# Kernel tuning notes

Hardware: AMD Instinct MI355X
Metric: run time of the kernel (lower is better)

## Reference

```python
import jax, jax.numpy as jnp
import numpy as np

L, T, R = 2, 2, 2          # layers, node types (0=user,1=movie), edge types
NU, NM, E = 50000, 10000, 500000
C, H, DPHI = 128, 4, 64
D = C // H                 # head dim = 32
SQRT_D = float(np.sqrt(D))


def setup_inputs() -> dict:
    key = jax.random.key(0)
    ks = jax.random.split(key, 16)
    s = 0.05
    src = jax.random.randint(ks[0], (E,), 0, NU)
    dst = jax.random.randint(ks[1], (E,), 0, NM)
    return {
        "user_emb": jax.random.normal(ks[2], (NU, C)) * 0.01,
        "movie_emb": jax.random.normal(ks[3], (NM, C)) * 0.01,
        "phi": jax.random.normal(ks[4], (NM, DPHI)),
        "meta_w": jax.random.normal(ks[5], (DPHI, C)) * s,
        "meta_b": jnp.zeros((C,)),
        "kw": jax.random.normal(ks[6], (L, T, C, C)) * s,
        "kb": jnp.zeros((L, T, C)),
        "qw": jax.random.normal(ks[7], (L, T, C, C)) * s,
        "qb": jnp.zeros((L, T, C)),
        "vw": jax.random.normal(ks[8], (L, T, C, C)) * s,
        "vb": jnp.zeros((L, T, C)),
        "a_rel": jax.random.normal(ks[9], (L, R, H, D, D)) * s,
        "m_rel": jax.random.normal(ks[10], (L, R, H, D, D)) * s,
        "p_rel": jnp.ones((L, R, H)),
        "ow": jax.random.normal(ks[11], (L, T, C, C)) * s,
        "ob": jnp.zeros((L, T, C)),
        "skip": jnp.ones((L, T)),
        "edge_index": jnp.stack([src, dst]),  # [2,E], row0=user idx, row1=movie idx
    }


def _segment_softmax(logits, seg, n):
    # logits: [E,H], seg: [E] destination node ids
    m = jax.ops.segment_max(logits, seg, num_segments=n)
    e = jnp.exp(logits - m[seg])
    s = jax.ops.segment_sum(e, seg, num_segments=n)
    return e / (s[seg] + 1e-16)


def _hgt_layer(xs, kw, kb, qw, qb, vw, vb, a_rel, m_rel, p_rel, ow, ob, skip, edge_index):
    ns = [x.shape[0] for x in xs]
    k = [(xs[t] @ kw[t] + kb[t]).reshape(ns[t], H, D) for t in range(T)]
    q = [(xs[t] @ qw[t] + qb[t]).reshape(ns[t], H, D) for t in range(T)]
    v = [(xs[t] @ vw[t] + vb[t]).reshape(ns[t], H, D) for t in range(T)]
    # edge types: r=0 user->movie, r=1 movie->user (reverse)
    etypes = [(0, 1, edge_index[0], edge_index[1]),
              (1, 0, edge_index[1], edge_index[0])]
    agg = [jnp.zeros((ns[t], C), dtype=xs[t].dtype) for t in range(T)]
    for r, (st, dt, src, dst) in enumerate(etypes):
        ke = jnp.einsum('nhd,hde->nhe', k[st], a_rel[r])   # per-edge-type key transform
        ve = jnp.einsum('nhd,hde->nhe', v[st], m_rel[r])
        logits = (q[dt][dst] * ke[src]).sum(-1) * p_rel[r] / SQRT_D   # [E,H]
        alpha = _segment_softmax(logits, dst, ns[dt])                  # [E,H]
        msg = (alpha[:, :, None] * ve[src]).reshape(-1, C)
        agg[dt] = agg[dt] + jax.ops.segment_sum(msg, dst, num_segments=ns[dt])
    out = []
    for t in range(T):
        o = jax.nn.gelu(agg[t]) @ ow[t] + ob[t]
        g = jax.nn.sigmoid(skip[t])
        out.append(g * o + (1.0 - g) * xs[t])
    return out


def reference(user_emb, movie_emb, phi, meta_w, meta_b, kw, kb, qw, qb, vw, vb,
              a_rel, m_rel, p_rel, ow, ob, skip, edge_index):
    xu = user_emb
    xm = movie_emb + phi @ meta_w + meta_b   # meta feature fusion on movie nodes
    xs = [xu, xm]
    for l in range(L):
        xs = _hgt_layer(xs, kw[l], kb[l], qw[l], qb[l], vw[l], vb[l],
                        a_rel[l], m_rel[l], p_rel[l], ow[l], ob[l], skip[l], edge_index)
    return (xs[0], xs[1])
```

## Files before the change

kernel.cpp:

```cpp
#include <hip/hip_runtime.h>
#include <hip/hip_bf16.h>

#define Cc 128
#define Hh 4
#define Dd 32
#define DPHI2 64
#define Ll 2
#define Tt 2
#define Rr 2

typedef __hip_bfloat16 bf16;
using short8 = __attribute__((ext_vector_type(8))) short;
using f32x4 = __attribute__((ext_vector_type(4))) float;
using f32x2 = __attribute__((ext_vector_type(2))) float;
typedef _Float16 h2 __attribute__((ext_vector_type(2)));
typedef __fp16 fp16x2 __attribute__((ext_vector_type(2)));

__device__ __forceinline__ unsigned short f2bf(float f) {
  union { float f; unsigned u; } v; v.f = f;
  unsigned r = v.u + 0x7fff + ((v.u >> 16) & 1);
  return (unsigned short)(r >> 16);
}
__device__ __forceinline__ h2 u2h(unsigned u) {
  union { unsigned u; h2 h; } v; v.u = u; return v.h;
}
__device__ __forceinline__ unsigned pkh(float a, float b) {
  union { unsigned u; fp16x2 h; } v;
  v.h = __builtin_amdgcn_cvt_pkrtz(a, b);
  return v.u;
}

__device__ __forceinline__ float fp8_decode1(unsigned char b) {
  unsigned u = b & 0x7f;
  float nrm = __builtin_bit_cast(float, (u << 20) + 0x3C000000u);
  float sub = (float)u * 0.001953125f;
  float v = (u >= 8) ? nrm : sub;
  return (b & 0x80) ? -v : v;
}
template <bool HI>
__device__ __forceinline__ f32x2 fp8x2f(unsigned w) {
#if __has_builtin(__builtin_amdgcn_cvt_pk_f32_fp8)
  return __builtin_amdgcn_cvt_pk_f32_fp8(w, HI);
#else
  unsigned b = HI ? (w >> 16) : (w & 0xffff);
  f32x2 r;
  r[0] = fp8_decode1((unsigned char)b);
  r[1] = fp8_decode1((unsigned char)(b >> 8));
  return r;
#endif
}
#if !__has_builtin(__builtin_amdgcn_cvt_pk_fp8_f32)
__device__ __forceinline__ unsigned char fp8_encode1(float f) {
  unsigned s = (__builtin_bit_cast(unsigned, f) >> 31) << 7;
  float a = fabsf(f);
  a = fminf(a, 448.f);
  unsigned char out;
  if (a < 0.0009765625f) {
    out = 0;
  } else if (a < 0.015625f) {
    out = (unsigned char)(a * 512.f + 0.5f);
  } else {
    unsigned bits = __builtin_bit_cast(unsigned, a);
    int e = (int)(bits >> 23) - 127;
    unsigned m = (bits >> 20) & 7;
    m += (bits >> 19) & 1;
    unsigned ee = (unsigned)(e + 7);
    if (m == 8) { m = 0; ee += 1; }
    if (ee > 15) { ee = 15; m = 6; }
    out = (unsigned char)((ee << 3) | m);
  }
  return out | (unsigned char)s;
}
#endif
__device__ __forceinline__ unsigned pk_fp8x4(float v0, float v1, float v2, float v3) {
#if __has_builtin(__builtin_amdgcn_cvt_pk_fp8_f32)
  int p = __builtin_amdgcn_cvt_pk_fp8_f32(v0, v1, 0, false);
  p = __builtin_amdgcn_cvt_pk_fp8_f32(v2, v3, p, true);
  return (unsigned)p;
#else
  return (unsigned)fp8_encode1(v0) | ((unsigned)fp8_encode1(v1) << 8) |
         ((unsigned)fp8_encode1(v2) << 16) | ((unsigned)fp8_encode1(v3) << 24);
#endif
}

__device__ __forceinline__ float dpp_add_xor1(float x) {
  int v = __builtin_amdgcn_update_dpp(0, __builtin_bit_cast(int, x), 0xB1, 0xF, 0xF, true);
  return x + __builtin_bit_cast(float, v);
}
__device__ __forceinline__ float dpp_add_xor2(float x) {
  int v = __builtin_amdgcn_update_dpp(0, __builtin_bit_cast(int, x), 0x4E, 0xF, 0xF, true);
  return x + __builtin_bit_cast(float, v);
}

__device__ __forceinline__ float gelu_tanh(float x) {
  float u = 0.7978845608028654f * (x + 0.044715f * x * x * x);
  float t = 1.f - 2.f / (__expf(2.f * u) + 1.f);
  return 0.5f * x * (1.f + t);
}

__device__ __forceinline__ void gload_lds16(const void* gsrc, void* lds) {
  __builtin_amdgcn_global_load_lds(
      (const __attribute__((address_space(1))) unsigned int*)gsrc,
      (__attribute__((address_space(3))) unsigned int*)lds, 16, 0, 0);
}

__global__ void hist_kernel(const int* __restrict__ src, const int* __restrict__ dst,
                            int E_, int NM_, int* cnt) {
  int e = blockIdx.x * 256 + threadIdx.x;
  if (e < E_) {
    atomicAdd(&cnt[dst[e]], 1);
    atomicAdd(&cnt[NM_ + src[e]], 1);
  }
}

__global__ __launch_bounds__(256) void scan_p1(const int* __restrict__ cnt, int n,
                                               int* __restrict__ psum) {
  int i0 = blockIdx.x * 1024 + threadIdx.x * 4;
  int s = 0;
#pragma unroll
  for (int j = 0; j < 4; ++j) {
    int i = i0 + j;
    if (i < n) s += cnt[i];
  }
#pragma unroll
  for (int off = 1; off < 64; off <<= 1) s += __shfl_xor(s, off, 64);
  __shared__ int wsum[4];
  if ((threadIdx.x & 63) == 0) wsum[threadIdx.x >> 6] = s;
  __syncthreads();
  if (threadIdx.x == 0) psum[blockIdx.x] = wsum[0] + wsum[1] + wsum[2] + wsum[3];
}
__global__ void scan_p2(int* psum, int nb) {
  if (threadIdx.x == 0 && blockIdx.x == 0) {
    int run = 0;
    for (int i = 0; i < nb; ++i) { int v = psum[i]; psum[i] = run; run += v; }
  }
}
__global__ __launch_bounds__(256) void scan_p3(const int* __restrict__ cnt, int n,
                                               const int* __restrict__ psum,
                                               int* __restrict__ rowptr) {
  __shared__ int sdata[256];
  int i0 = blockIdx.x * 1024 + threadIdx.x * 4;
  int a0 = (i0 + 0 < n) ? cnt[i0 + 0] : 0;
  int a1 = (i0 + 1 < n) ? cnt[i0 + 1] : 0;
  int a2 = (i0 + 2 < n) ? cnt[i0 + 2] : 0;
  int a3 = (i0 + 3 < n) ? cnt[i0 + 3] : 0;
  int s = a0 + a1 + a2 + a3;
  sdata[threadIdx.x] = s;
  __syncthreads();
  for (int off = 1; off < 256; off <<= 1) {
    int t = ((int)threadIdx.x >= off) ? sdata[threadIdx.x - off] : 0;
    __syncthreads();
    sdata[threadIdx.x] += t;
    __syncthreads();
  }
  int run = psum[blockIdx.x] + sdata[threadIdx.x] - s;
  if (i0 + 0 < n) rowptr[i0 + 1] = run + a0;
  if (i0 + 1 < n) rowptr[i0 + 2] = run + a0 + a1;
  if (i0 + 2 < n) rowptr[i0 + 3] = run + a0 + a1 + a2;
  if (i0 + 3 < n) rowptr[i0 + 4] = run + s;
  if (blockIdx.x == 0 && threadIdx.x == 0) rowptr[0] = 0;
}

__global__ void scatter_kernel(const int* __restrict__ src, const int* __restrict__ dst, int E_,
                               const int* __restrict__ rowptr, int* cnt,
                               int* __restrict__ srcAll, int NU_, int NM_) {
  int e = blockIdx.x * 256 + threadIdx.x;
  if (e < E_) {
    int s = src[e], d = dst[e];
    int pm = rowptr[d] + atomicAdd(&cnt[d], 1);
    srcAll[pm] = s << 8;
    int pu = rowptr[NM_ + s] + atomicAdd(&cnt[NM_ + s], 1);
    srcAll[pu] = (NU_ + d) << 8;
  }
}

__global__ __launch_bounds__(128) void prep_weights(
    const float* __restrict__ kw, const float* __restrict__ kb,
    const float* __restrict__ qw, const float* __restrict__ qb,
    const float* __restrict__ vw, const float* __restrict__ vb,
    const float* __restrict__ a_rel, const float* __restrict__ m_rel,
    const float* __restrict__ p_rel, const float* __restrict__ ow,
    const float* __restrict__ ob,
    unsigned short* __restrict__ WT, float* __restrict__ bQKV,
    unsigned short* __restrict__ OWT, float* __restrict__ bO) {
  int g = blockIdx.x;
  int lt = blockIdx.y;
  int l = lt >> 1, t = lt & 1, r = t;
  int k = threadIdx.x;
  const float inv_sqrt_d = 0.17677669529663687f;
  const float QSCALE = 1.4426950408889634f / 256.f;
  const float KSCALE = 256.f;
  const float VSCALE = 256.f;
  float val, bval;
  if (g < 128) {
    val = qw[((size_t)lt * Cc + k) * Cc + g] * QSCALE;
    bval = qb[(size_t)lt * Cc + g] * QSCALE;
  } else if (g < 384) {
    int isV = (g >= 256);
    int n = g - (isV ? 256 : 128);
    int h = n >> 5, e = n & 31;
    const float* W = (isV ? vw : kw) + (size_t)lt * Cc * Cc;
    const float* bb = (isV ? vb : kb) + (size_t)lt * Cc;
    const float* Ah = (isV ? m_rel : a_rel) + (((size_t)l * Rr + r) * Hh + h) * Dd * Dd;
    float s = 0.f, sb = 0.f;
    for (int d = 0; d < Dd; ++d) {
      float ae = Ah[d * Dd + e];
      s += W[(size_t)k * Cc + h * Dd + d] * ae;
      sb += bb[h * Dd + d] * ae;
    }
    float scale = isV ? VSCALE : p_rel[((size_t)l * Rr + r) * Hh + h] * inv_sqrt_d * KSCALE;
    val = s * scale;
    bval = sb * scale;
  } else {
    int n = g - 384;
    val = ow[((size_t)lt * Cc + k) * Cc + n];
    bval = ob[(size_t)lt * Cc + n];
  }
  if (g < 384) {
    WT[((size_t)lt * 384 + g) * Cc + k] = f2bf(val);
    if (k == 0) bQKV[(size_t)lt * 384 + g] = bval;
  } else {
    OWT[((size_t)lt * Cc + (g - 384)) * Cc + k] = f2bf(val);
    if (k == 0) bO[(size_t)lt * Cc + (g - 384)] = bval;
  }
}

__global__ void init_kernel(const float* __restrict__ ue, const float* __restrict__ me,
                            const float* __restrict__ phi, const float* __restrict__ mw,
                            const float* __restrict__ mb,
                            float* __restrict__ xout, unsigned short* __restrict__ Xb,
                            int NU_, int NM_) {
  int i = blockIdx.x * 256 + threadIdx.x;
  int totalU = NU_ * Cc;
  if (i < totalU) {
    float v = ue[i];
    xout[i] = v;
    Xb[i] = f2bf(v);
  } else {
    int j = i - totalU;
    if (j >= NM_ * Cc) return;
    int m = j >> 7, c = j & 127;
    float s = me[j] + mb[c];
    const float* ph = phi + (size_t)m * DPHI2;
    for (int d = 0; d < DPHI2; ++d) s += ph[d] * mw[d * Cc + c];
    xout[i] = s;
    Xb[i] = f2bf(s);
  }
}

template <int NCH, int MODE>
__global__ __launch_bounds__(256, 2) void mfma_gemm(
    int NBU_, int NU_, int NM_,
    const bf16* __restrict__ Abase,
    const bf16* __restrict__ WTl, const float* __restrict__ biasl,
    char* __restrict__ Qc, char* __restrict__ KVc,
    float* __restrict__ xout, unsigned short* __restrict__ Xb,
    const float* __restrict__ skipl) {
  __shared__ char Bs[2][16384];
  int bx = blockIdx.x;
  int t, row0, M, base;
  if (bx < NBU_) { t = 0; row0 = bx * 128; M = NU_; base = 0; }
  else { t = 1; row0 = (bx - NBU_) * 128; M = NM_; base = NU_; }
  const char* BT = (const char*)(WTl + (size_t)t * (NCH * 64) * Cc);
  const float* bias = biasl + (size_t)t * (NCH * 64);
  int wid = threadIdx.x >> 6, lane = threadIdx.x & 63;
  int rw = row0 + wid * 32;
  bool wact = rw < M;
  int lr = lane & 15, lk8 = (lane >> 4) * 8;

  auto stage = [&](int ch, int buf) {
    const char* src = BT + (size_t)ch * 16384;
#pragma unroll
    for (int j = 0; j < 4; ++j) {
      int u = wid * 4 + j;
      int d = u * 1024 + lane * 16;
      int g = d ^ (((d >> 8) & 7) << 4);
      gload_lds16(src + g, &Bs[buf][u * 1024]);
    }
  };

  short8 a[2][4];
#pragma unroll
  for (int mt = 0; mt < 2; ++mt) {
    int r = rw + mt * 16 + lr;
    const bf16* ap = Abase + (size_t)(base + r) * Cc + lk8;
#pragma unroll
    for (int kk = 0; kk < 4; ++kk) {
      short8 v = {};
      if (wact && r < M) v = *(const short8*)(ap + kk * 32);
      a[mt][kk] = v;
    }
  }
  float g = 0.f;
  if (MODE == 1) g = 1.f / (1.f + __expf(-skipl[t]));

  stage(0, 0);
#pragma unroll
  for (int ch = 0; ch < NCH; ++ch) {
    int buf = ch & 1;
    __syncthreads();
    if (ch + 1 < NCH) stage(ch + 1, buf ^ 1);
    short8 b[4][4];
#pragma unroll
    for (int nt = 0; nt < 4; ++nt) {
      int r = nt * 16 + lr;
#pragma unroll
      for (int kk = 0; kk < 4; ++kk) {
        int a0 = r * 256 + (lk8 + kk * 32) * 2;
        b[nt][kk] = *(const short8*)(&Bs[buf][a0 ^ ((r & 7) << 4)]);
      }
    }
    f32x4 acc[2][4];
#pragma unroll
    for (int mt = 0; mt < 2; ++mt)
#pragma unroll
      for (int nt = 0; nt < 4; ++nt) acc[mt][nt] = (f32x4){0.f, 0.f, 0.f, 0.f};
#pragma unroll
    for (int kk = 0; kk < 4; ++kk)
#pragma unroll
      for (int mt = 0; mt < 2; ++mt)
#pragma unroll
        for (int nt = 0; nt < 4; ++nt)
          acc[mt][nt] = __builtin_amdgcn_mfma_f32_16x16x32_bf16(
              b[nt][kk], a[mt][kk], acc[mt][nt], 0, 0, 0);
    if (!wact) continue;
#pragma unroll
    for (int mt = 0; mt < 2; ++mt) {
      int r = rw + mt * 16 + lr;
      if (r >= M) continue;
      size_t grow = (size_t)(base + r);
#pragma unroll
      for (int nt = 0; nt < 4; ++nt) {
        int cb = ch * 64 + nt * 16 + 4 * (lane >> 4);
        float4 b4 = *(const float4*)&bias[cb];
        float v0 = acc[mt][nt][0] + b4.x;
        float v1 = acc[mt][nt][1] + b4.y;
        float v2 = acc[mt][nt][2] + b4.z;
        float v3 = acc[mt][nt][3] + b4.w;
        if (MODE == 0) {
          if (cb < Cc) {
            uint2 pk;
            pk.x = pkh(v0, v1); pk.y = pkh(v2, v3);
            *(uint2*)(Qc + grow * 256 + cb * 2) = pk;
          } else {
            int c = cb - 128;
            int isv = c >> 7; c &= 127;
            int off = (c >> 3) * 16 + (c & 7) + isv * 8;
            unsigned pk = pk_fp8x4(v0, v1, v2, v3);
            *(unsigned*)(KVc + grow * 256 + off) = pk;
          }
        } else {
          float* xp = xout + grow * Cc + cb;
          float4 old = *(const float4*)xp;
          float n0 = g * v0 + (1.f - g) * old.x;
          float n1 = g * v1 + (1.f - g) * old.y;
          float n2 = g * v2 + (1.f - g) * old.z;
          float n3 = g * v3 + (1.f - g) * old.w;
          *(float4*)xp = make_float4(n0, n1, n2, n3);
          uint2 pk;
          pk.x = (unsigned)f2bf(n0) | ((unsigned)f2bf(n1) << 16);
          pk.y = (unsigned)f2bf(n2) | ((unsigned)f2bf(n3) << 16);
          *(uint2*)(Xb + grow * Cc + cb) = pk;
        }
      }
    }
  }
}

__global__ __launch_bounds__(256) void agg_kernel(
    const int* __restrict__ rowptr, const int* __restrict__ srcAll,
    const char* __restrict__ Qc, const char* __restrict__ KVc,
    unsigned short* __restrict__ AGGb, int NM_, int NU_) {
  int wid = threadIdx.x >> 6, lane = threadIdx.x & 63;
  int sub = lane & 15, eo = lane >> 4;
  int NT_ = NM_ + NU_;
  int W = (blockIdx.x * 4 + wid) * 4 + eo;
  bool active = W < NT_;
  int Wc = active ? W : NT_ - 1;
  int beg = rowptr[Wc];
  int end = active ? rowptr[Wc + 1] : beg;
  int dnode = (Wc < NM_) ? (NU_ + Wc) : (Wc - NM_);
  int myoff = sub * 16;
  uint4 qv = *(const uint4*)(Qc + (size_t)dnode * 256 + myoff);
  float qf0, qf1, qf2, qf3, qf4, qf5, qf6, qf7;
  {
    h2 t0 = u2h(qv.x), t1 = u2h(qv.y), t2 = u2h(qv.z), t3 = u2h(qv.w);
    qf0 = (float)t0[0]; qf1 = (float)t0[1];
    qf2 = (float)t1[0]; qf3 = (float)t1[1];
    qf4 = (float)t2[0]; qf5 = (float)t2[1];
    qf6 = (float)t3[0]; qf7 = (float)t3[1];
  }
  float acc0 = 0.f, acc1 = 0.f, acc2 = 0.f, acc3 = 0.f;
  float acc4 = 0.f, acc5 = 0.f, acc6 = 0.f, acc7 = 0.f;
  float denom = 0.f;
  const char* KVp = KVc + myoff;

#define CONSUME(KV, WVALID)                                                       \
  {                                                                               \
    f32x2 k01 = fp8x2f<false>((KV).x), k23 = fp8x2f<true>((KV).x);                \
    f32x2 k45 = fp8x2f<false>((KV).y), k67 = fp8x2f<true>((KV).y);                \
    float pA = qf0 * k01[0] + qf1 * k01[1] + qf2 * k23[0] + qf3 * k23[1];         \
    float pB = qf4 * k45[0] + qf5 * k45[1] + qf6 * k67[0] + qf7 * k67[1];         \
    float p = pA + pB;                                                            \
    p = dpp_add_xor1(p);                                                          \
    p = dpp_add_xor2(p);                                                          \
    float w = (WVALID) ? exp2f(p) : 0.f;                                          \
    denom += w;                                                                   \
    f32x2 v01 = fp8x2f<false>((KV).z), v23 = fp8x2f<true>((KV).z);                \
    f32x2 v45 = fp8x2f<false>((KV).w), v67 = fp8x2f<true>((KV).w);                \
    acc0 += w * v01[0]; acc1 += w * v01[1];                                       \
    acc2 += w * v23[0]; acc3 += w * v23[1];                                       \
    acc4 += w * v45[0]; acc5 += w * v45[1];                                       \
    acc6 += w * v67[0]; acc7 += w * v67[1];                                       \
  }

  for (int e = beg; __any(e < end); e += 2) {
    bool v0 = e < end, v1 = (e + 1) < end;
    int so0 = srcAll[v0 ? e : 0];
    int so1 = srcAll[v1 ? (e + 1) : 0];
    uint4 kv0 = *(const uint4*)(KVp + (size_t)(unsigned)so0);
    uint4 kv1 = *(const uint4*)(KVp + (size_t)(unsigned)so1);
    CONSUME(kv0, v0)
    CONSUME(kv1, v1)
  }
#undef CONSUME

  if (active) {
    float inv = 1.f / (denom + 1e-16f) * 0.00390625f;
    float o0 = gelu_tanh(acc0 * inv);
    float o1 = gelu_tanh(acc1 * inv);
    float o2 = gelu_tanh(acc2 * inv);
    float o3 = gelu_tanh(acc3 * inv);
    float o4 = gelu_tanh(acc4 * inv);
    float o5 = gelu_tanh(acc5 * inv);
    float o6 = gelu_tanh(acc6 * inv);
    float o7 = gelu_tanh(acc7 * inv);
    uint4 pk;
    pk.x = (unsigned)f2bf(o0) | ((unsigned)f2bf(o1) << 16);
    pk.y = (unsigned)f2bf(o2) | ((unsigned)f2bf(o3) << 16);
    pk.z = (unsigned)f2bf(o4) | ((unsigned)f2bf(o5) << 16);
    pk.w = (unsigned)f2bf(o6) | ((unsigned)f2bf(o7) << 16);
    *(uint4*)(AGGb + (size_t)dnode * Cc + sub * 8) = pk;
  }
}

extern "C" void kernel_launch(void* const* d_in, const int* in_sizes, int n_in,
                              void* d_out, int out_size, void* d_ws, size_t ws_size,
                              hipStream_t stream) {
  const float* user_emb = (const float*)d_in[0];
  const float* movie_emb = (const float*)d_in[1];
  const float* phi = (const float*)d_in[2];
  const float* meta_w = (const float*)d_in[3];
  const float* meta_b = (const float*)d_in[4];
  const float* kw = (const float*)d_in[5];
  const float* kb = (const float*)d_in[6];
  const float* qw = (const float*)d_in[7];
  const float* qb = (const float*)d_in[8];
  const float* vw = (const float*)d_in[9];
  const float* vb = (const float*)d_in[10];
  const float* a_rel = (const float*)d_in[11];
  const float* m_rel = (const float*)d_in[12];
  const float* p_rel = (const float*)d_in[13];
  const float* ow = (const float*)d_in[14];
  const float* ob = (const float*)d_in[15];
  const float* skip = (const float*)d_in[16];
  const int* eidx = (const int*)d_in[17];

  int NU = in_sizes[0] / Cc;
  int NM = in_sizes[1] / Cc;
  int E_ = in_sizes[17] / 2;
  int NT = NU + NM;
  const int* esrc = eidx;
  const int* edst = eidx + E_;

  char* ws = (char*)d_ws;
  size_t off = 0;
  auto alloc = [&](size_t bytes) -> char* {
    char* p = ws + off;
    off = (off + bytes + 255) & ~(size_t)255;
    return p;
  };
  char* Qc = alloc((size_t)NT * 256);
  char* KVc = alloc((size_t)NT * 256);
  unsigned short* Xb = (unsigned short*)alloc((size_t)NT * Cc * 2);
  unsigned short* AGGb = (unsigned short*)alloc((size_t)NT * Cc * 2);
  unsigned short* WT = (unsigned short*)alloc((size_t)Ll * Tt * 384 * Cc * 2);
  unsigned short* OWT = (unsigned short*)alloc((size_t)Ll * Tt * Cc * Cc * 2);
  float* bQKV = (float*)alloc((size_t)Ll * Tt * 384 * 4);
  float* bO = (float*)alloc((size_t)Ll * Tt * Cc * 4);
  int* rowptr = (int*)alloc((size_t)(NT + 1) * 4);
  int* srcAll = (int*)alloc((size_t)2 * E_ * 4);
  int* cnt = (int*)alloc((size_t)NT * 4);
  int* psum = (int*)alloc((size_t)256 * 4);
  float* xout = (float*)d_out;

  int nblk = (NT + 1023) / 1024;

  hipMemsetAsync(cnt, 0, (size_t)NT * 4, stream);
  hist_kernel<<<(E_ + 255) / 256, 256, 0, stream>>>(esrc, edst, E_, NM, cnt);
  scan_p1<<<nblk, 256, 0, stream>>>(cnt, NT, psum);
  scan_p2<<<1, 64, 0, stream>>>(psum, nblk);
  scan_p3<<<nblk, 256, 0, stream>>>(cnt, NT, psum, rowptr);
  hipMemsetAsync(cnt, 0, (size_t)NT * 4, stream);
  scatter_kernel<<<(E_ + 255) / 256, 256, 0, stream>>>(esrc, edst, E_, rowptr, cnt,
                                                       srcAll, NU, NM);

  prep_weights<<<dim3(512, 4), 128, 0, stream>>>(kw, kb, qw, qb, vw, vb, a_rel, m_rel,
                                                 p_rel, ow, ob, WT, bQKV, OWT, bO);
  init_kernel<<<(NT * Cc + 255) / 256, 256, 0, stream>>>(user_emb, movie_emb, phi,
                                                         meta_w, meta_b, xout, Xb, NU, NM);

  int NBU = (NU + 127) / 128;
  int NBM = (NM + 127) / 128;
  dim3 ggrid(NBU + NBM);
  int nagg = (NT + 15) / 16;
  for (int l = 0; l < Ll; ++l) {
    mfma_gemm<6, 0><<<ggrid, 256, 0, stream>>>(
        NBU, NU, NM, (const bf16*)Xb, (const bf16*)(WT + (size_t)l * 2 * 384 * Cc),
        bQKV + (size_t)l * 2 * 384, Qc, KVc, nullptr, nullptr, nullptr);
    agg_kernel<<<nagg, 256, 0, stream>>>(rowptr, srcAll, Qc, KVc, AGGb, NM, NU);
    mfma_gemm<2, 1><<<ggrid, 256, 0, stream>>>(
        NBU, NU, NM, (const bf16*)AGGb, (const bf16*)(OWT + (size_t)l * 2 * Cc * Cc),
        bO + (size_t)l * 2 * Cc, nullptr, nullptr, xout, Xb, skip + (size_t)l * 2);
  }
}
```

Before: 328.6 us.

## Merge setup kernels and fold CSR scatter into first QKV GEMM launch

Combines the histogram, weight preparation and embedding init kernels into one launch. The histogram now records each edge's atomic slot offset, so the later scatter needs no second memset or second round of atomics. That scatter runs as extra blocks appended to the first layer's QKV GEMM grid. The aim is to cut launch count and serialization in the setup phase. The cost is two extra E-sized offset buffers and extra blocks in the GEMM grid that may contend with it.

```diff
diff --git a/kernel.cpp b/kernel.cpp
--- a/kernel.cpp
+++ b/kernel.cpp
@@ -104,12 +104,87 @@
       (__attribute__((address_space(3))) unsigned int*)lds, 16, 0, 0);
 }
 
-__global__ void hist_kernel(const int* __restrict__ src, const int* __restrict__ dst,
-                            int E_, int NM_, int* cnt) {
-  int e = blockIdx.x * 256 + threadIdx.x;
-  if (e < E_) {
-    atomicAdd(&cnt[dst[e]], 1);
-    atomicAdd(&cnt[NM_ + src[e]], 1);
+__global__ __launch_bounds__(256) void setup_kernel(
+    const int* __restrict__ esrc, const int* __restrict__ edst, int E_, int NM_, int NU_,
+    int* __restrict__ cnt, int* __restrict__ eoffm, int* __restrict__ eoffu,
+    const float* __restrict__ kw, const float* __restrict__ kb,
+    const float* __restrict__ qw, const float* __restrict__ qb,
+    const float* __restrict__ vw, const float* __restrict__ vb,
+    const float* __restrict__ a_rel, const float* __restrict__ m_rel,
+    const float* __restrict__ p_rel, const float* __restrict__ ow,
+    const float* __restrict__ ob,
+    unsigned short* __restrict__ WT, float* __restrict__ bQKV,
+    unsigned short* __restrict__ OWT, float* __restrict__ bO,
+    const float* __restrict__ ue, const float* __restrict__ me,
+    const float* __restrict__ phi, const float* __restrict__ mw,
+    const float* __restrict__ mb,
+    float* __restrict__ xout, unsigned short* __restrict__ Xb,
+    int HB, int PB) {
+  int b = blockIdx.x;
+  if (b < HB) {
+    int e = b * 256 + threadIdx.x;
+    if (e < E_) {
+      eoffm[e] = atomicAdd(&cnt[edst[e]], 1);
+      eoffu[e] = atomicAdd(&cnt[NM_ + esrc[e]], 1);
+    }
+    return;
+  }
+  if (b < HB + PB) {
+    int idx = (b - HB) * 2 + (threadIdx.x >> 7);
+    int g = idx >> 2, lt = idx & 3;
+    int l = lt >> 1, t = lt & 1, r = t;
+    int k = threadIdx.x & 127;
+    const float inv_sqrt_d = 0.17677669529663687f;
+    const float QSCALE = 1.4426950408889634f / 256.f;
+    float val, bval;
+    if (g < 128) {
+      val = qw[((size_t)lt * Cc + k) * Cc + g] * QSCALE;
+      bval = qb[(size_t)lt * Cc + g] * QSCALE;
+    } else if (g < 384) {
+      int isV = (g >= 256);
+      int n = g - (isV ? 256 : 128);
+      int h = n >> 5, e = n & 31;
+      const float* W = (isV ? vw : kw) + (size_t)lt * Cc * Cc;
+      const float* bb = (isV ? vb : kb) + (size_t)lt * Cc;
+      const float* Ah = (isV ? m_rel : a_rel) + (((size_t)l * Rr + r) * Hh + h) * Dd * Dd;
+      float s = 0.f, sb = 0.f;
+      for (int d = 0; d < Dd; ++d) {
+        float ae = Ah[d * Dd + e];
+        s += W[(size_t)k * Cc + h * Dd + d] * ae;
+        sb += bb[h * Dd + d] * ae;
+      }
+      float scale = isV ? 256.f : p_rel[((size_t)l * Rr + r) * Hh + h] * inv_sqrt_d * 256.f;
+      val = s * scale;
+      bval = sb * scale;
+    } else {
+      int n = g - 384;
+      val = ow[((size_t)lt * Cc + k) * Cc + n];
+      bval = ob[(size_t)lt * Cc + n];
+    }
+    if (g < 384) {
+      WT[((size_t)lt * 384 + g) * Cc + k] = f2bf(val);
+      if (k == 0) bQKV[(size_t)lt * 384 + g] = bval;
+    } else {
+      OWT[((size_t)lt * Cc + (g - 384)) * Cc + k] = f2bf(val);
+      if (k == 0) bO[(size_t)lt * Cc + (g - 384)] = bval;
+    }
+    return;
+  }
+  int i = (b - HB - PB) * 256 + threadIdx.x;
+  int totalU = NU_ * Cc;
+  if (i < totalU) {
+    float v = ue[i];
+    xout[i] = v;
+    Xb[i] = f2bf(v);
+  } else {
+    int j = i - totalU;
+    if (j >= NM_ * Cc) return;
+    int m = j >> 7, c = j & 127;
+    float s = me[j] + mb[c];
+    const float* ph = phi + (size_t)m * DPHI2;
+    for (int d = 0; d < DPHI2; ++d) s += ph[d] * mw[d * Cc + c];
+    xout[i] = s;
+    Xb[i] = f2bf(s);
   }
 }
 
@@ -161,93 +236,6 @@
   if (blockIdx.x == 0 && threadIdx.x == 0) rowptr[0] = 0;
 }
 
-__global__ void scatter_kernel(const int* __restrict__ src, const int* __restrict__ dst, int E_,
-                               const int* __restrict__ rowptr, int* cnt,
-                               int* __restrict__ srcAll, int NU_, int NM_) {
-  int e = blockIdx.x * 256 + threadIdx.x;
-  if (e < E_) {
-    int s = src[e], d = dst[e];
-    int pm = rowptr[d] + atomicAdd(&cnt[d], 1);
-    srcAll[pm] = s << 8;
-    int pu = rowptr[NM_ + s] + atomicAdd(&cnt[NM_ + s], 1);
-    srcAll[pu] = (NU_ + d) << 8;
-  }
-}
-
-__global__ __launch_bounds__(128) void prep_weights(
-    const float* __restrict__ kw, const float* __restrict__ kb,
-    const float* __restrict__ qw, const float* __restrict__ qb,
-    const float* __restrict__ vw, const float* __restrict__ vb,
-    const float* __restrict__ a_rel, const float* __restrict__ m_rel,
-    const float* __restrict__ p_rel, const float* __restrict__ ow,
-    const float* __restrict__ ob,
-    unsigned short* __restrict__ WT, float* __restrict__ bQKV,
-    unsigned short* __restrict__ OWT, float* __restrict__ bO) {
-  int g = blockIdx.x;
-  int lt = blockIdx.y;
-  int l = lt >> 1, t = lt & 1, r = t;
-  int k = threadIdx.x;
-  const float inv_sqrt_d = 0.17677669529663687f;
-  const float QSCALE = 1.4426950408889634f / 256.f;
-  const float KSCALE = 256.f;
-  const float VSCALE = 256.f;
-  float val, bval;
-  if (g < 128) {
-    val = qw[((size_t)lt * Cc + k) * Cc + g] * QSCALE;
-    bval = qb[(size_t)lt * Cc + g] * QSCALE;
-  } else if (g < 384) {
-    int isV = (g >= 256);
-    int n = g - (isV ? 256 : 128);
-    int h = n >> 5, e = n & 31;
-    const float* W = (isV ? vw : kw) + (size_t)lt * Cc * Cc;
-    const float* bb = (isV ? vb : kb) + (size_t)lt * Cc;
-    const float* Ah = (isV ? m_rel : a_rel) + (((size_t)l * Rr + r) * Hh + h) * Dd * Dd;
-    float s = 0.f, sb = 0.f;
-    for (int d = 0; d < Dd; ++d) {
-      float ae = Ah[d * Dd + e];
-      s += W[(size_t)k * Cc + h * Dd + d] * ae;
-      sb += bb[h * Dd + d] * ae;
-    }
-    float scale = isV ? VSCALE : p_rel[((size_t)l * Rr + r) * Hh + h] * inv_sqrt_d * KSCALE;
-    val = s * scale;
-    bval = sb * scale;
-  } else {
-    int n = g - 384;
-    val = ow[((size_t)lt * Cc + k) * Cc + n];
-    bval = ob[(size_t)lt * Cc + n];
-  }
-  if (g < 384) {
-    WT[((size_t)lt * 384 + g) * Cc + k] = f2bf(val);
-    if (k == 0) bQKV[(size_t)lt * 384 + g] = bval;
-  } else {
-    OWT[((size_t)lt * Cc + (g - 384)) * Cc + k] = f2bf(val);
-    if (k == 0) bO[(size_t)lt * Cc + (g - 384)] = bval;
-  }
-}
-
-__global__ void init_kernel(const float* __restrict__ ue, const float* __restrict__ me,
-                            const float* __restrict__ phi, const float* __restrict__ mw,
-                            const float* __restrict__ mb,
-                            float* __restrict__ xout, unsigned short* __restrict__ Xb,
-                            int NU_, int NM_) {
-  int i = blockIdx.x * 256 + threadIdx.x;
-  int totalU = NU_ * Cc;
-  if (i < totalU) {
-    float v = ue[i];
-    xout[i] = v;
-    Xb[i] = f2bf(v);
-  } else {
-    int j = i - totalU;
-    if (j >= NM_ * Cc) return;
-    int m = j >> 7, c = j & 127;
-    float s = me[j] + mb[c];
-    const float* ph = phi + (size_t)m * DPHI2;
-    for (int d = 0; d < DPHI2; ++d) s += ph[d] * mw[d * Cc + c];
-    xout[i] = s;
-    Xb[i] = f2bf(s);
-  }
-}
-
 template <int NCH, int MODE>
 __global__ __launch_bounds__(256, 2) void mfma_gemm(
     int NBU_, int NU_, int NM_,
@@ -255,8 +243,20 @@
     const bf16* __restrict__ WTl, const float* __restrict__ biasl,
     char* __restrict__ Qc, char* __restrict__ KVc,
     float* __restrict__ xout, unsigned short* __restrict__ Xb,
-    const float* __restrict__ skipl) {
+    const float* __restrict__ skipl,
+    int GB, const int* __restrict__ esrc, const int* __restrict__ edst, int E_,
+    const int* __restrict__ rowptr, const int* __restrict__ eoffm,
+    const int* __restrict__ eoffu, int* __restrict__ srcAll) {
   __shared__ char Bs[2][16384];
+  if ((int)blockIdx.x >= GB) {
+    int e = ((int)blockIdx.x - GB) * 256 + threadIdx.x;
+    if (e < E_) {
+      int s = esrc[e], d = edst[e];
+      srcAll[rowptr[d] + eoffm[e]] = s << 8;
+      srcAll[rowptr[NM_ + s] + eoffu[e]] = (NU_ + d) << 8;
+    }
+    return;
+  }
   int bx = blockIdx.x;
   int t, row0, M, base;
   if (bx < NBU_) { t = 0; row0 = bx * 128; M = NU_; base = 0; }
@@ -490,37 +490,41 @@
   float* bO = (float*)alloc((size_t)Ll * Tt * Cc * 4);
   int* rowptr = (int*)alloc((size_t)(NT + 1) * 4);
   int* srcAll = (int*)alloc((size_t)2 * E_ * 4);
+  int* eoffm = (int*)alloc((size_t)E_ * 4);
+  int* eoffu = (int*)alloc((size_t)E_ * 4);
   int* cnt = (int*)alloc((size_t)NT * 4);
   int* psum = (int*)alloc((size_t)256 * 4);
   float* xout = (float*)d_out;
 
   int nblk = (NT + 1023) / 1024;
+  int HB = (E_ + 255) / 256;
+  int PB = 1024;
+  int IB = (NT * Cc + 255) / 256;
 
   hipMemsetAsync(cnt, 0, (size_t)NT * 4, stream);
-  hist_kernel<<<(E_ + 255) / 256, 256, 0, stream>>>(esrc, edst, E_, NM, cnt);
+  setup_kernel<<<HB + PB + IB, 256, 0, stream>>>(
+      esrc, edst, E_, NM, NU, cnt, eoffm, eoffu,
+      kw, kb, qw, qb, vw, vb, a_rel, m_rel, p_rel, ow, ob,
+      WT, bQKV, OWT, bO,
+      user_emb, movie_emb, phi, meta_w, meta_b, xout, Xb, HB, PB);
   scan_p1<<<nblk, 256, 0, stream>>>(cnt, NT, psum);
   scan_p2<<<1, 64, 0, stream>>>(psum, nblk);
   scan_p3<<<nblk, 256, 0, stream>>>(cnt, NT, psum, rowptr);
-  hipMemsetAsync(cnt, 0, (size_t)NT * 4, stream);
-  scatter_kernel<<<(E_ + 255) / 256, 256, 0, stream>>>(esrc, edst, E_, rowptr, cnt,
-                                                       srcAll, NU, NM);
-
-  prep_weights<<<dim3(512, 4), 128, 0, stream>>>(kw, kb, qw, qb, vw, vb, a_rel, m_rel,
-                                                 p_rel, ow, ob, WT, bQKV, OWT, bO);
-  init_kernel<<<(NT * Cc + 255) / 256, 256, 0, stream>>>(user_emb, movie_emb, phi,
-                                                         meta_w, meta_b, xout, Xb, NU, NM);
 
   int NBU = (NU + 127) / 128;
   int NBM = (NM + 127) / 128;
-  dim3 ggrid(NBU + NBM);
+  int GB = NBU + NBM;
   int nagg = (NT + 15) / 16;
   for (int l = 0; l < Ll; ++l) {
-    mfma_gemm<6, 0><<<ggrid, 256, 0, stream>>>(
+    int extra = (l == 0) ? HB : 0;
+    mfma_gemm<6, 0><<<GB + extra, 256, 0, stream>>>(
         NBU, NU, NM, (const bf16*)Xb, (const bf16*)(WT + (size_t)l * 2 * 384 * Cc),
-        bQKV + (size_t)l * 2 * 384, Qc, KVc, nullptr, nullptr, nullptr);
+        bQKV + (size_t)l * 2 * 384, Qc, KVc, nullptr, nullptr, nullptr,
+        GB, esrc, edst, (l == 0) ? E_ : 0, rowptr, eoffm, eoffu, srcAll);
     agg_kernel<<<nagg, 256, 0, stream>>>(rowptr, srcAll, Qc, KVc, AGGb, NM, NU);
-    mfma_gemm<2, 1><<<ggrid, 256, 0, stream>>>(
+    mfma_gemm<2, 1><<<GB, 256, 0, stream>>>(
         NBU, NU, NM, (const bf16*)AGGb, (const bf16*)(OWT + (size_t)l * 2 * Cc * Cc),
-        bO + (size_t)l * 2 * Cc, nullptr, nullptr, xout, Xb, skip + (size_t)l * 2);
-  }
-}
+        bO + (size_t)l * 2 * Cc, nullptr, nullptr, xout, Xb, skip + (size_t)l * 2,
+        GB, nullptr, nullptr, 0, nullptr, nullptr, nullptr, nullptr);
+  }
+}
```

New measurement: 285.2 us. -13.2%, faster.
